# Optimization experiments

Hardware: AMD Instinct MI355X
Metric: run time of the kernel (lower is better)

Reference implementation:

```python
import jax, jax.numpy as jnp
import numpy as np

B, EVI, L, H, K, NL = 16, 5, 128, 768, 21, 3
SIGMA = 0.1

def _kernel_mus(n):
    mu = [1.0]
    bin_size = 2.0 / (n - 1)
    mu.append(1 - bin_size / 2)
    for i in range(1, n - 1):
        mu.append(mu[i] - bin_size)
    return mu

MU = np.asarray(_kernel_mus(K), dtype=np.float32)                      # [K]
SIG = np.asarray([0.001] + [SIGMA] * (K - 1), dtype=np.float32)        # [K]


def setup_inputs() -> dict:
    key = jax.random.key(0)
    ks = jax.random.split(key, 8)
    std = 0.02
    inputs_hiddens = jax.random.normal(ks[0], (B, EVI, L, H), jnp.float32)
    inputs = jax.random.normal(ks[1], (B, EVI, H), jnp.float32)
    # mask_text: valid tokens with CLS (position 0) zeroed, as in torch forward
    mask_text = jnp.ones((B, EVI, L), jnp.float32).at[:, :, 0].set(0.0)
    seg = (jnp.arange(L) >= L // 2).astype(jnp.float32)  # first half = claim, second = evidence
    mask_claim = (1.0 - seg) * mask_text
    mask_evidence = seg * mask_text
    return {
        "inputs_hiddens": inputs_hiddens,
        "inputs": inputs,
        "mask_text": mask_text,
        "mask_claim": mask_claim,
        "mask_evidence": mask_evidence,
        "W_att": jax.random.normal(ks[2], (K, 1), jnp.float32) * std,
        "b_att": jnp.zeros((1,), jnp.float32),
        "W_sel": jax.random.normal(ks[3], (K, 1), jnp.float32) * std,
        "b_sel": jnp.zeros((1,), jnp.float32),
        "gat_W1": jax.random.normal(ks[4], (2 * H, 128), jnp.float32) * std,
        "gat_b1": jnp.zeros((128,), jnp.float32),
        "gat_W2": jax.random.normal(ks[5], (128, 1), jnp.float32) * std,
        "gat_b2": jnp.zeros((1,), jnp.float32),
        "inf_W": jax.random.normal(ks[6], (2 * H, NL), jnp.float32) * std,
        "inf_b": jnp.zeros((NL,), jnp.float32),
    }


def _l2norm(x):
    # F.normalize(p=2, dim=-1) with eps=1e-12
    return x / jnp.maximum(jnp.linalg.norm(x, axis=-1, keepdims=True), 1e-12)


def _kernel_pool(sim, attn_d):
    # sim: [N, Lq, Ld]; attn_d: [N, Ld]  ->  [N, Lq, K]
    # exp(-(sim - mu)^2 / (2 sigma^2)) masked by doc attention, summed over doc tokens
    pv = jnp.exp(-((sim[..., None] - MU) ** 2) / (2.0 * SIG ** 2)) * attn_d[:, None, :, None]
    return pv.sum(axis=2)


def _intersect_att(qn, dn, attn_q, attn_d, W_att, b_att):
    # token-level attention scores over q tokens: [N, Lq]
    sim = jnp.einsum('nqh,ndh->nqd', qn, dn)
    lp = jnp.log(jnp.maximum(_kernel_pool(sim, attn_d), 1e-10))  # [N, Lq, K]
    lp = (lp @ W_att + b_att)[..., 0]                            # [N, Lq]
    lp = jnp.where(attn_q == 0.0, -1e4, lp)
    return jax.nn.softmax(lp, axis=1)


def _intersect_sel(qn, dn, attn_q, attn_d, W_sel, b_sel):
    # per-pair evidence selection logit: [N, 1]
    sim = jnp.einsum('nqh,ndh->nqd', qn, dn)
    lp = jnp.log(jnp.maximum(_kernel_pool(sim, attn_d), 1e-10)) * attn_q[..., None] * 0.01
    lp = lp.sum(axis=1) / (attn_q.sum(axis=1, keepdims=True) + 1e-10)  # [N, K]
    return lp @ W_sel + b_sel


def _gat(x, W1, b1, W2, b2):
    # proj_gat: Linear(2H,128) -> ReLU -> Linear(128,1)
    return jnp.maximum(x @ W1 + b1, 0.0) @ W2 + b2


def reference(inputs_hiddens, inputs, mask_text, mask_claim, mask_evidence,
              W_att, b_att, W_sel, b_sel, gat_W1, gat_b1, gat_W2, gat_b2,
              inf_W, inf_b):
    hid = inputs_hiddens                          # [B, EVI, L, H]
    hn = _l2norm(hid)
    hn_flat = hn.reshape(-1, L, H)

    # evidence selection prior over EVI pieces
    sel = _intersect_sel(hn_flat, hn_flat,
                         mask_claim.reshape(-1, L), mask_evidence.reshape(-1, L),
                         W_sel, b_sel)
    select_prob = jax.nn.softmax(sel.reshape(B, EVI, 1), axis=1)

    att_de = []
    for i in range(EVI):  # fixed small structural loop
        own_n = hn[:, i]                           # [B, L, H]
        own_mask = mask_text[:, i]                 # [B, L]
        dn = jnp.broadcast_to(own_n[:, None], (B, EVI, L, H)).reshape(-1, L, H)
        dm = jnp.broadcast_to(own_mask[:, None], (B, EVI, L)).reshape(-1, L)
        att = _intersect_att(hn_flat, dn, mask_evidence.reshape(-1, L), dm, W_att, b_att)
        att = att.reshape(B, EVI, L, 1)
        denoise = (att * hid).sum(axis=2)          # [B, EVI, H]
        own_inp = jnp.broadcast_to(inputs[:, i:i + 1], (B, EVI, H))
        w_de = jax.nn.softmax(_gat(jnp.concatenate([own_inp, denoise], -1),
                                   gat_W1, gat_b1, gat_W2, gat_b2), axis=1)  # [B, EVI, 1]
        att_de.append((denoise * w_de).sum(axis=1))  # [B, H]

    att_de = jnp.stack(att_de, axis=1)             # [B, EVI, H]
    feats = jnp.concatenate([inputs, att_de], axis=-1)  # [B, EVI, 2H]
    class_prob = jax.nn.softmax(feats @ inf_W + inf_b, axis=2)
    prob = jnp.log((select_prob * class_prob).sum(axis=1))  # [B, NL]
    return prob
```

## Files before the change

### kernel.cpp

```cpp
#include <hip/hip_runtime.h>
#include <math.h>

#define NB 16
#define NE 5
#define LL 128
#define HH 768
#define NK 21
#define NCLS 3
#define NN (NB*NE)

typedef float f32x4 __attribute__((ext_vector_type(4)));
typedef float f32x8 __attribute__((ext_vector_type(8)));
typedef short s16x8 __attribute__((ext_vector_type(8)));

__device__ __forceinline__ short bf16rne(float f) {
    union { float f; unsigned u; } c; c.f = f;
    unsigned u = c.u;
    unsigned r = (u + 0x7FFFu + ((u >> 16) & 1u)) >> 16;
    return (short)r;
}
__device__ __forceinline__ float sum8(f32x8 x) {
    return ((x[0] + x[1]) + (x[2] + x[3])) + ((x[4] + x[5]) + (x[6] + x[7]));
}
__device__ __forceinline__ f32x8 exp2v(f32x8 x) {
    f32x8 r;
    r[0] = exp2f(x[0]); r[1] = exp2f(x[1]); r[2] = exp2f(x[2]); r[3] = exp2f(x[3]);
    r[4] = exp2f(x[4]); r[5] = exp2f(x[5]); r[6] = exp2f(x[6]); r[7] = exp2f(x[7]);
    return r;
}
__device__ __forceinline__ f32x8 mk8(float4 a, float4 b) {
    f32x8 r;
    r[0] = a.x; r[1] = a.y; r[2] = a.z; r[3] = a.w;
    r[4] = b.x; r[5] = b.y; r[6] = b.z; r[7] = b.w;
    return r;
}
__device__ __forceinline__ float dot4(float4 a, float4 b) {
    return fmaf(a.x, b.x, fmaf(a.y, b.y, fmaf(a.z, b.z, a.w * b.w)));
}

__global__ __launch_bounds__(256) void k_prep(const float* __restrict__ hid,
                                              short* __restrict__ hswz,
                                              const float* __restrict__ W1,
                                              float* __restrict__ w1t) {
    __shared__ float sT[64][65];
    const int tid = threadIdx.x;
    if (blockIdx.x >= 640) {
        const int bb = blockIdx.x - 640;
        const int tI = bb >> 1, jI = bb & 1;
        #pragma unroll
        for (int i = 0; i < 16; ++i) {
            const int r = (tid >> 6) + i * 4, c = tid & 63;
            sT[r][c] = W1[(size_t)(tI * 64 + r) * 128 + jI * 64 + c];
        }
        __syncthreads();
        #pragma unroll
        for (int i = 0; i < 16; ++i) {
            const int r = (tid >> 6) + i * 4, c = tid & 63;
            w1t[(size_t)(jI * 64 + r) * 1536 + tI * 64 + c] = sT[c][r];
        }
        return;
    }
    const int n = blockIdx.x >> 3, slab = blockIdx.x & 7;
    const int l = tid & 63, w = tid >> 6;
    float* sInv = &sT[0][0];
    #pragma unroll
    for (int rr = 0; rr < 4; ++rr) {
        const int lr = w * 4 + rr;
        const int row = slab * 16 + lr;
        const float4* rp = reinterpret_cast<const float4*>(hid + ((size_t)n * LL + row) * HH);
        float4 a = rp[l], b = rp[l + 64], c = rp[l + 128];
        float ss = a.x*a.x + a.y*a.y + a.z*a.z + a.w*a.w
                 + b.x*b.x + b.y*b.y + b.z*b.z + b.w*b.w
                 + c.x*c.x + c.y*c.y + c.z*c.z + c.w*c.w;
        #pragma unroll
        for (int o = 32; o > 0; o >>= 1) ss += __shfl_xor(ss, o, 64);
        if (l == 0) sInv[lr] = 1.0f / fmaxf(sqrtf(ss), 1e-12f);
    }
    __syncthreads();
    const float* base = hid + (size_t)n * LL * HH;
    s16x8* dst = reinterpret_cast<s16x8*>(hswz) + (size_t)n * 12288;
    #pragma unroll
    for (int i = 0; i < 6; ++i) {
        const int uid = i * 256 + tid;
        const int s = uid >> 6, sub = uid & 63;
        const int r15 = sub >> 2, kc = sub & 3;
        const int row = slab * 16 + r15;
        const int k0 = s * 32 + kc * 8;
        const float4* p = reinterpret_cast<const float4*>(base + (size_t)row * HH + k0);
        float4 v0 = p[0], v1 = p[1];
        const float inv = sInv[r15];
        s16x8 h;
        h[0] = bf16rne(v0.x * inv); h[1] = bf16rne(v0.y * inv);
        h[2] = bf16rne(v0.z * inv); h[3] = bf16rne(v0.w * inv);
        h[4] = bf16rne(v1.x * inv); h[5] = bf16rne(v1.y * inv);
        h[6] = bf16rne(v1.z * inv); h[7] = bf16rne(v1.w * inv);
        dst[(size_t)s * 512 + slab * 64 + kc * 16 + r15] = h;
    }
}

__global__ __launch_bounds__(256, 3) void k_simpool(
    const short* __restrict__ hswz,
    const float* __restrict__ mask_text, const float* __restrict__ mask_claim,
    const float* __restrict__ mask_evidence,
    const float* __restrict__ W_att, const float* __restrict__ b_att,
    const float* __restrict__ W_sel,
    float* __restrict__ attw, float2* __restrict__ dselPart)
{
    const int bid = blockIdx.x;
    const int b = bid & 15, rest = bid >> 4;
    const int pair = rest >> 1, qh = rest & 1;
    const int e = pair / NE, ep = pair - e * NE;
    const int nq = b * NE + e, nd = b * NE + ep;
    const bool diag = (e == ep);
    const int tid = threadIdx.x, lane = tid & 63, w = tid >> 6;
    const int lx = lane & 15, lg = lane >> 4;

    __shared__ s16x8 sB[1024];
    __shared__ __align__(16) float sMT[LL];
    __shared__ __align__(16) float sMEd[LL];
    __shared__ float sMEq[64], sMCq[64], sSel[64];
    __shared__ float sWA[NK], sWS[NK], sCK[NK];

    if (tid < 128) {
        sMT[tid]  = mask_text[nd * LL + tid];
        sMEd[tid] = mask_evidence[nd * LL + tid];
    } else if (tid < 192) {
        const int q = tid - 128;
        sMEq[q] = mask_evidence[nq * LL + qh * 64 + q];
        sMCq[q] = mask_claim[nq * LL + qh * 64 + q];
    } else if (tid < 192 + NK) {
        sWA[tid - 192] = W_att[tid - 192] * 0.69314718f;
    } else if (tid < 213 + NK) {
        sWS[tid - 213] = W_sel[tid - 213] * 0.69314718f;
    } else if (tid < 254) {
        const int k = tid - 233;
        const float kk = (float)(k - 1);
        sCK[k] = exp2f(fmaf(kk, 13.7056029f, fmaf(kk * kk, -0.72134752f, -32.0f)));
    } else if (tid == 254) {
        sCK[0] = 1.0f;
    }

    const s16x8* gA = reinterpret_cast<const s16x8*>(hswz) + (size_t)nq * 12288;
    const s16x8* gB = reinterpret_cast<const s16x8*>(hswz) + (size_t)nd * 12288;

    {
        s16x8 p0 = gB[tid], p1 = gB[tid + 256], p2 = gB[tid + 512], p3 = gB[tid + 768];
        sB[tid] = p0; sB[tid + 256] = p1; sB[tid + 512] = p2; sB[tid + 768] = p3;
    }
    s16x8 b0 = gB[1024 + tid], b1 = gB[1024 + tid + 256],
          b2 = gB[1024 + tid + 512], b3 = gB[1024 + tid + 768];
    const int arow = (qh * 4 + w) * 64 + lane;
    s16x8 aC0 = gA[arow];
    s16x8 aC1 = gA[512 + arow];
    s16x8 aN0 = gA[1024 + arow];
    s16x8 aN1 = gA[1024 + 512 + arow];

    f32x4 acc[8];
    #pragma unroll
    for (int nj = 0; nj < 8; ++nj) acc[nj] = (f32x4){0.f, 0.f, 0.f, 0.f};

    for (int s = 0; s < 12; ++s) {
        __syncthreads();
        #pragma unroll
        for (int nj = 0; nj < 8; ++nj)
            acc[nj] = __builtin_amdgcn_mfma_f32_16x16x32_bf16(aC0, sB[nj * 64 + lane], acc[nj], 0, 0, 0);
        #pragma unroll
        for (int nj = 0; nj < 8; ++nj)
            acc[nj] = __builtin_amdgcn_mfma_f32_16x16x32_bf16(aC1, sB[512 + nj * 64 + lane], acc[nj], 0, 0, 0);
        if (s < 11) {
            __syncthreads();
            sB[tid] = b0; sB[tid + 256] = b1; sB[tid + 512] = b2; sB[tid + 768] = b3;
            aC0 = aN0; aC1 = aN1;
            if (s < 10) {
                const s16x8* gBs = gB + (s + 2) * 1024;
                b0 = gBs[tid]; b1 = gBs[tid + 256];
                b2 = gBs[tid + 512]; b3 = gBs[tid + 768];
                aN0 = gA[(s + 2) * 1024 + arow];
                aN1 = gA[(s + 2) * 1024 + 512 + arow];
            }
        }
    }

    float* sS = reinterpret_cast<float*>(sB);
    const int rloc = (w << 3) | (lane & 7);
    const int slice = lane >> 3;
    const int xr = lane & 7;
    const float bAtt = b_att[0];
    const size_t obase = ((size_t)ep * NN + nq) * LL + qh * 64;

    #pragma unroll
    for (int ph = 0; ph < 2; ++ph) {
        __syncthreads();
        if ((w >> 1) == ph) {
            const int wl = w & 1;
            #pragma unroll
            for (int nj = 0; nj < 8; ++nj) {
                const int col = nj * 16 + lx;
                #pragma unroll
                for (int r = 0; r < 4; ++r) {
                    const int row = wl * 16 + lg * 4 + r;
                    const int unit = (col >> 2) ^ (row & 7);
                    sS[row * 128 + unit * 4 + (col & 3)] = acc[nj][r];
                }
            }
        }
        __syncthreads();

        const float4* rp4 = reinterpret_cast<const float4*>(sS + rloc * 128);
        float pk[NK], vkk[NK];
        #pragma unroll
        for (int k = 0; k < NK; ++k) { pk[k] = 0.f; vkk[k] = 0.f; }

        #pragma unroll
        for (int c = 0; c < 2; ++c) {
            const float4 qa = rp4[(slice * 4 + c * 2) ^ xr];
            const float4 qb = rp4[(slice * 4 + c * 2 + 1) ^ xr];
            const f32x8 s = mk8(qa, qb);
            const int j0 = slice * 16 + c * 8;
            const f32x8 m = mk8(*reinterpret_cast<const float4*>(&sMT[j0]),
                                *reinterpret_cast<const float4*>(&sMT[j0 + 4]));
            f32x8 d = s - 1.0f;
            const f32x8 g = exp2v(d * d * -721347.52f);
            pk[0] += sum8(m * g);
            const f32x8 t = exp2v(s * -14.4269504f);
            d = s - 0.95f;
            const f32x8 P = exp2v(d * d * -72.134752f + 32.0f);
            f32x8 u = m * P;
            pk[1] += sum8(u);
            #pragma unroll
            for (int k = 2; k <= 20; ++k) { u *= t; pk[k] += sum8(u); }
            if (diag) {
                const f32x8 me = mk8(*reinterpret_cast<const float4*>(&sMEd[j0]),
                                     *reinterpret_cast<const float4*>(&sMEd[j0 + 4]));
                f32x8 uv = me * P;
                vkk[0] += sum8(me * g);
                vkk[1] += sum8(uv);
                #pragma unroll
                for (int k = 2; k <= 20; ++k) { uv *= t; vkk[k] += sum8(uv); }
            }
        }
        #pragma unroll
        for (int k = 0; k < NK; ++k) {
            pk[k] += __shfl_xor(pk[k], 8, 64);
            pk[k] += __shfl_xor(pk[k], 16, 64);
            pk[k] += __shfl_xor(pk[k], 32, 64);
        }
        if (diag) {
            #pragma unroll
            for (int k = 0; k < NK; ++k) {
                vkk[k] += __shfl_xor(vkk[k], 8, 64);
                vkk[k] += __shfl_xor(vkk[k], 16, 64);
                vkk[k] += __shfl_xor(vkk[k], 32, 64);
            }
        }
        const int grow = ph * 32 + rloc;
        float lgt = bAtt;
        #pragma unroll
        for (int k = 0; k < NK; ++k)
            lgt = fmaf(sWA[k], log2f(fmaxf(pk[k] * sCK[k], 1e-10f)), lgt);
        if (slice == 0)
            attw[obase + grow] = (sMEq[grow] == 0.0f) ? -10000.0f : lgt;
        if (diag) {
            float rv = 0.f;
            #pragma unroll
            for (int k = 0; k < NK; ++k)
                rv = fmaf(sWS[k], log2f(fmaxf(vkk[k] * sCK[k], 1e-10f)), rv);
            if (slice == 0) sSel[grow] = sMCq[grow] * rv;
        }
    }
    if (diag) {
        __syncthreads();
        if (tid < 64) {
            float su = sSel[tid], ms = sMCq[tid];
            #pragma unroll
            for (int o = 32; o > 0; o >>= 1) {
                su += __shfl_xor(su, o, 64);
                ms += __shfl_xor(ms, o, 64);
            }
            if (tid == 0) dselPart[nq * 2 + qh] = make_float2(su, ms);
        }
    }
}

__global__ __launch_bounds__(256) void k_denoise(
    const float* __restrict__ hid, const float* __restrict__ attw,
    float* __restrict__ denoi)
{
    const int blk = blockIdx.x;
    const int nq = blk / 3, ch = blk - nq * 3;
    const int tid = threadIdx.x, l = tid & 63, w = tid >> 6;
    __shared__ float sA[NE][LL];
    for (int ep = w; ep < NE; ep += 4) {
        const float* ap = attw + ((size_t)ep * NN + nq) * LL;
        float a0 = ap[l], a1 = ap[l + 64];
        float m = fmaxf(a0, a1);
        #pragma unroll
        for (int o = 32; o > 0; o >>= 1) m = fmaxf(m, __shfl_xor(m, o, 64));
        float e0 = __expf(a0 - m), e1 = __expf(a1 - m);
        float s = e0 + e1;
        #pragma unroll
        for (int o = 32; o > 0; o >>= 1) s += __shfl_xor(s, o, 64);
        float inv = 1.0f / s;
        sA[ep][l] = e0 * inv;
        sA[ep][l + 64] = e1 * inv;
    }
    __syncthreads();
    const int h = ch * 256 + tid;
    const float* hp = hid + (size_t)nq * LL * HH + h;
    float a0 = 0.f, a1 = 0.f, a2 = 0.f, a3 = 0.f, a4 = 0.f;
    #pragma unroll 8
    for (int q = 0; q < LL; ++q) {
        float x = hp[(size_t)q * HH];
        a0 = fmaf(sA[0][q], x, a0);
        a1 = fmaf(sA[1][q], x, a1);
        a2 = fmaf(sA[2][q], x, a2);
        a3 = fmaf(sA[3][q], x, a3);
        a4 = fmaf(sA[4][q], x, a4);
    }
    denoi[((size_t)0 * NN + nq) * HH + h] = a0;
    denoi[((size_t)1 * NN + nq) * HH + h] = a1;
    denoi[((size_t)2 * NN + nq) * HH + h] = a2;
    denoi[((size_t)3 * NN + nq) * HH + h] = a3;
    denoi[((size_t)4 * NN + nq) * HH + h] = a4;
}

__global__ __launch_bounds__(256) void k_gat2(
    const float* __restrict__ inputs, const float* __restrict__ denoise,
    const float* __restrict__ w1t, const float* __restrict__ b1,
    const float* __restrict__ W2, float* __restrict__ part)
{
    const int wid = blockIdx.x * 4 + (threadIdx.x >> 6);
    const int l = threadIdx.x & 63;
    const int jp = wid & 63;
    const int po = wid >> 6;
    const int j0 = jp * 2, j1 = j0 + 1;
    const int pb = po * 8;

    const float4* wc0 = reinterpret_cast<const float4*>(w1t + (size_t)j0 * 1536) + l;
    const float4* wc1 = reinterpret_cast<const float4*>(w1t + (size_t)j1 * 1536) + l;
    const float4* fin[8]; const float4* fde[8];
    #pragma unroll
    for (int u = 0; u < 8; ++u) {
        const int p = pb + u;
        const int i = p / NN; const int n2 = p - i * NN; const int bb = n2 / NE;
        fin[u] = reinterpret_cast<const float4*>(inputs + ((size_t)bb * NE + i) * HH) + l;
        fde[u] = reinterpret_cast<const float4*>(denoise + (size_t)p * HH) + l;
    }
    float a0[8], a1[8];
    #pragma unroll
    for (int u = 0; u < 8; ++u) { a0[u] = 0.f; a1[u] = 0.f; }

    #pragma unroll
    for (int it = 0; it < 3; ++it) {
        const float4 w0v = wc0[it * 64], w1v = wc1[it * 64];
        #pragma unroll
        for (int u = 0; u < 8; ++u) {
            const float4 f = fin[u][it * 64];
            a0[u] += dot4(f, w0v);
            a1[u] += dot4(f, w1v);
        }
    }
    #pragma unroll
    for (int it = 0; it < 3; ++it) {
        const float4 w0v = wc0[192 + it * 64], w1v = wc1[192 + it * 64];
        #pragma unroll
        for (int u = 0; u < 8; ++u) {
            const float4 f = fde[u][it * 64];
            a0[u] += dot4(f, w0v);
            a1[u] += dot4(f, w1v);
        }
    }
    #pragma unroll
    for (int u = 0; u < 8; ++u) {
        #pragma unroll
        for (int o = 32; o > 0; o >>= 1) {
            a0[u] += __shfl_xor(a0[u], o, 64);
            a1[u] += __shfl_xor(a1[u], o, 64);
        }
    }
    const float bb0 = b1[j0], bb1 = b1[j1], w20 = W2[j0], w21 = W2[j1];
    if (l == 0) {
        #pragma unroll
        for (int u = 0; u < 8; ++u) {
            float v = fmaxf(a0[u] + bb0, 0.f) * w20 + fmaxf(a1[u] + bb1, 0.f) * w21;
            part[(size_t)(pb + u) * 64 + jp] = v;
        }
    }
}

__global__ __launch_bounds__(256) void k_logits(
    const float* __restrict__ inputs, const float* __restrict__ denoise,
    const float* __restrict__ part, const float* __restrict__ inf_W,
    const float* __restrict__ inf_b, float* __restrict__ logi)
{
    const int bid = blockIdx.x;
    const int b = bid / NE, i = bid - b * NE;
    const int tid = threadIdx.x, l = tid & 63, wv = tid >> 6;
    __shared__ float sG[NE];
    for (int e2 = wv; e2 < NE; e2 += 4) {
        float v = part[(size_t)(i * NN + b * NE + e2) * 64 + l];
        #pragma unroll
        for (int o = 32; o > 0; o >>= 1) v += __shfl_xor(v, o, 64);
        if (l == 0) sG[e2] = v;
    }
    __syncthreads();
    float g0 = sG[0], g1 = sG[1], g2 = sG[2], g3 = sG[3], g4 = sG[4];
    float mm = fmaxf(fmaxf(fmaxf(g0, g1), fmaxf(g2, g3)), g4);
    float w0 = __expf(g0 - mm), w1 = __expf(g1 - mm), w2 = __expf(g2 - mm);
    float w3 = __expf(g3 - mm), w4 = __expf(g4 - mm);
    float inv = 1.0f / (w0 + w1 + w2 + w3 + w4);
    w0 *= inv; w1 *= inv; w2 *= inv; w3 *= inv; w4 *= inv;

    float p0 = 0.f, p1 = 0.f, p2 = 0.f;
    const float* xin = inputs + ((size_t)b * NE + i) * HH;
    const float* de = denoise + ((size_t)i * NN + b * NE) * HH;
    #pragma unroll
    for (int it = 0; it < 3; ++it) {
        int t = it * 256 + tid;
        float f = xin[t];
        p0 += f * inf_W[t * 3]; p1 += f * inf_W[t * 3 + 1]; p2 += f * inf_W[t * 3 + 2];
    }
    #pragma unroll
    for (int it = 0; it < 3; ++it) {
        int h = it * 256 + tid;
        float a = w0 * de[h] + w1 * de[HH + h] + w2 * de[2 * HH + h]
                + w3 * de[3 * HH + h] + w4 * de[4 * HH + h];
        int t = HH + h;
        p0 += a * inf_W[t * 3]; p1 += a * inf_W[t * 3 + 1]; p2 += a * inf_W[t * 3 + 2];
    }
    #pragma unroll
    for (int o = 32; o > 0; o >>= 1) {
        p0 += __shfl_xor(p0, o, 64);
        p1 += __shfl_xor(p1, o, 64);
        p2 += __shfl_xor(p2, o, 64);
    }
    __shared__ float red[4][NCLS];
    if (l == 0) { red[wv][0] = p0; red[wv][1] = p1; red[wv][2] = p2; }
    __syncthreads();
    if (tid < NCLS) {
        logi[bid * NCLS + tid] = red[0][tid] + red[1][tid] + red[2][tid] + red[3][tid]
                               + inf_b[tid];
    }
}

__global__ __launch_bounds__(64) void k_combine(
    const float2* __restrict__ dselPart, const float* __restrict__ b_sel,
    const float* __restrict__ logi, float* __restrict__ out)
{
    const int b = threadIdx.x;
    if (b >= NB) return;
    const float bs = b_sel[0];
    float d0, d1, d2, d3, d4;
#define DSEL(I, D) { float2 pa = dselPart[(b * NE + (I)) * 2], pb = dselPart[(b * NE + (I)) * 2 + 1]; \
                     (D) = bs + 0.01f * (pa.x + pb.x) / ((pa.y + pb.y) + 1e-10f); }
    DSEL(0, d0) DSEL(1, d1) DSEL(2, d2) DSEL(3, d3) DSEL(4, d4)
#undef DSEL
    float m = fmaxf(fmaxf(fmaxf(d0, d1), fmaxf(d2, d3)), d4);
    float s0 = __expf(d0 - m), s1 = __expf(d1 - m), s2 = __expf(d2 - m);
    float s3 = __expf(d3 - m), s4 = __expf(d4 - m);
    float sinv = 1.0f / (s0 + s1 + s2 + s3 + s4);
    float sp0 = s0 * sinv, sp1 = s1 * sinv, sp2 = s2 * sinv, sp3 = s3 * sinv, sp4 = s4 * sinv;
    float acc0 = 0.f, acc1 = 0.f, acc2 = 0.f;
#define CMB(I, SP) { \
        float l0 = logi[(b * NE + (I)) * NCLS], l1 = logi[(b * NE + (I)) * NCLS + 1], \
              l2 = logi[(b * NE + (I)) * NCLS + 2]; \
        float mm = fmaxf(fmaxf(l0, l1), l2); \
        float e0 = __expf(l0 - mm), e1 = __expf(l1 - mm), e2 = __expf(l2 - mm); \
        float si = 1.0f / (e0 + e1 + e2); \
        acc0 += (SP) * e0 * si; acc1 += (SP) * e1 * si; acc2 += (SP) * e2 * si; }
    CMB(0, sp0) CMB(1, sp1) CMB(2, sp2) CMB(3, sp3) CMB(4, sp4)
#undef CMB
    out[b * NCLS + 0] = logf(acc0);
    out[b * NCLS + 1] = logf(acc1);
    out[b * NCLS + 2] = logf(acc2);
}

extern "C" void kernel_launch(void* const* d_in, const int* in_sizes, int n_in,
                              void* d_out, int out_size, void* d_ws, size_t ws_size,
                              hipStream_t stream) {
    (void)in_sizes; (void)n_in; (void)out_size; (void)ws_size;
    const float* hid           = (const float*)d_in[0];
    const float* inputs        = (const float*)d_in[1];
    const float* mask_text     = (const float*)d_in[2];
    const float* mask_claim    = (const float*)d_in[3];
    const float* mask_evidence = (const float*)d_in[4];
    const float* W_att  = (const float*)d_in[5];
    const float* b_att  = (const float*)d_in[6];
    const float* W_sel  = (const float*)d_in[7];
    const float* b_sel  = (const float*)d_in[8];
    const float* gat_W1 = (const float*)d_in[9];
    const float* gat_b1 = (const float*)d_in[10];
    const float* gat_W2 = (const float*)d_in[11];
    const float* gat_b2 = (const float*)d_in[12];
    const float* inf_W  = (const float*)d_in[13];
    const float* inf_b  = (const float*)d_in[14];
    (void)gat_b2;

    short* hswz  = (short*)d_ws;
    float* denoi = (float*)((char*)d_ws + 15728640);
    float* attw  = denoi + 307200;
    float2* dselPart = (float2*)(attw + 51200);
    float* w1t   = (float*)(dselPart + 160);
    float* part  = w1t + 196608;
    float* logi  = part + 25600;

    k_prep<<<688, 256, 0, stream>>>(hid, hswz, gat_W1, w1t);
    k_simpool<<<800, 256, 0, stream>>>(hswz, mask_text, mask_claim, mask_evidence,
                                       W_att, b_att, W_sel, attw, dselPart);
    k_denoise<<<NN * 3, 256, 0, stream>>>(hid, attw, denoi);
    k_gat2<<<800, 256, 0, stream>>>(inputs, denoi, w1t, gat_b1, gat_W2, part);
    k_logits<<<NN, 256, 0, stream>>>(inputs, denoi, part, inf_W, inf_b, logi);
    k_combine<<<1, 64, 0, stream>>>(dselPart, b_sel, logi, (float*)d_out);
}
```

Before: 92.77 us.

## Retile simpool MFMA to 2x4 wave grid with double-buffered LDS; fuse logits+combine

The similarity GEMM in k_simpool now uses a 2x2 wave layout where each wave computes 2 row tiles by 4 column tiles, so every B fragment read from LDS feeds two MFMAs. K is split into 24 steps of 32 with a double-buffered 16KB LDS B tile, which needs one barrier per step instead of two. The launch-bounds occupancy hint drops from 3 to 2 blocks per CU. Separately, k_logits and k_combine are merged into one 16-block kernel, removing a launch, at the cost of less parallelism in the final stage.

```diff
diff --git a/kernel.cpp b/kernel.cpp
--- a/kernel.cpp
+++ b/kernel.cpp
@@ -98,7 +98,7 @@
     }
 }
 
-__global__ __launch_bounds__(256, 3) void k_simpool(
+__global__ __launch_bounds__(256, 2) void k_simpool(
     const short* __restrict__ hswz,
     const float* __restrict__ mask_text, const float* __restrict__ mask_claim,
     const float* __restrict__ mask_evidence,
@@ -114,8 +114,9 @@
     const bool diag = (e == ep);
     const int tid = threadIdx.x, lane = tid & 63, w = tid >> 6;
     const int lx = lane & 15, lg = lane >> 4;
-
-    __shared__ s16x8 sB[1024];
+    const int rw = w & 1, cw = w >> 1;
+
+    __shared__ s16x8 sB[2][512];
     __shared__ __align__(16) float sMT[LL];
     __shared__ __align__(16) float sMEd[LL];
     __shared__ float sMEq[64], sMCq[64], sSel[64];
@@ -143,41 +144,41 @@
     const s16x8* gA = reinterpret_cast<const s16x8*>(hswz) + (size_t)nq * 12288;
     const s16x8* gB = reinterpret_cast<const s16x8*>(hswz) + (size_t)nd * 12288;
 
-    {
-        s16x8 p0 = gB[tid], p1 = gB[tid + 256], p2 = gB[tid + 512], p3 = gB[tid + 768];
-        sB[tid] = p0; sB[tid + 256] = p1; sB[tid + 512] = p2; sB[tid + 768] = p3;
-    }
-    s16x8 b0 = gB[1024 + tid], b1 = gB[1024 + tid + 256],
-          b2 = gB[1024 + tid + 512], b3 = gB[1024 + tid + 768];
-    const int arow = (qh * 4 + w) * 64 + lane;
-    s16x8 aC0 = gA[arow];
-    s16x8 aC1 = gA[512 + arow];
-    s16x8 aN0 = gA[1024 + arow];
-    s16x8 aN1 = gA[1024 + 512 + arow];
-
-    f32x4 acc[8];
-    #pragma unroll
-    for (int nj = 0; nj < 8; ++nj) acc[nj] = (f32x4){0.f, 0.f, 0.f, 0.f};
-
-    for (int s = 0; s < 12; ++s) {
-        __syncthreads();
-        #pragma unroll
-        for (int nj = 0; nj < 8; ++nj)
-            acc[nj] = __builtin_amdgcn_mfma_f32_16x16x32_bf16(aC0, sB[nj * 64 + lane], acc[nj], 0, 0, 0);
-        #pragma unroll
-        for (int nj = 0; nj < 8; ++nj)
-            acc[nj] = __builtin_amdgcn_mfma_f32_16x16x32_bf16(aC1, sB[512 + nj * 64 + lane], acc[nj], 0, 0, 0);
-        if (s < 11) {
+    const int rt0 = (qh * 4 + rw * 2) * 64;
+    const int rt1 = rt0 + 64;
+    const int cb  = cw * 256;
+
+    sB[0][tid] = gB[tid];
+    sB[0][tid + 256] = gB[tid + 256];
+    s16x8 a0 = gA[rt0 + lane], a1 = gA[rt1 + lane];
+
+    f32x4 acc[2][4];
+    #pragma unroll
+    for (int mi = 0; mi < 2; ++mi)
+        #pragma unroll
+        for (int j = 0; j < 4; ++j) acc[mi][j] = (f32x4){0.f, 0.f, 0.f, 0.f};
+
+    __syncthreads();
+
+    for (int s = 0; s < 24; ++s) {
+        const int cur = s & 1;
+        s16x8 nB0, nB1, n0, n1;
+        if (s < 23) {
+            const s16x8* gBs = gB + (s + 1) * 512;
+            nB0 = gBs[tid]; nB1 = gBs[tid + 256];
+            const s16x8* gAs = gA + (s + 1) * 512;
+            n0 = gAs[rt0 + lane]; n1 = gAs[rt1 + lane];
+        }
+        #pragma unroll
+        for (int j = 0; j < 4; ++j) {
+            s16x8 bf = sB[cur][cb + j * 64 + lane];
+            acc[0][j] = __builtin_amdgcn_mfma_f32_16x16x32_bf16(a0, bf, acc[0][j], 0, 0, 0);
+            acc[1][j] = __builtin_amdgcn_mfma_f32_16x16x32_bf16(a1, bf, acc[1][j], 0, 0, 0);
+        }
+        if (s < 23) {
+            sB[1 - cur][tid] = nB0; sB[1 - cur][tid + 256] = nB1;
+            a0 = n0; a1 = n1;
             __syncthreads();
-            sB[tid] = b0; sB[tid + 256] = b1; sB[tid + 512] = b2; sB[tid + 768] = b3;
-            aC0 = aN0; aC1 = aN1;
-            if (s < 10) {
-                const s16x8* gBs = gB + (s + 2) * 1024;
-                b0 = gBs[tid]; b1 = gBs[tid + 256];
-                b2 = gBs[tid + 512]; b3 = gBs[tid + 768];
-                aN0 = gA[(s + 2) * 1024 + arow];
-                aN1 = gA[(s + 2) * 1024 + 512 + arow];
-            }
         }
     }
 
@@ -191,16 +192,18 @@
     #pragma unroll
     for (int ph = 0; ph < 2; ++ph) {
         __syncthreads();
-        if ((w >> 1) == ph) {
-            const int wl = w & 1;
+        if (rw == ph) {
             #pragma unroll
-            for (int nj = 0; nj < 8; ++nj) {
-                const int col = nj * 16 + lx;
+            for (int mi = 0; mi < 2; ++mi) {
                 #pragma unroll
-                for (int r = 0; r < 4; ++r) {
-                    const int row = wl * 16 + lg * 4 + r;
-                    const int unit = (col >> 2) ^ (row & 7);
-                    sS[row * 128 + unit * 4 + (col & 3)] = acc[nj][r];
+                for (int j = 0; j < 4; ++j) {
+                    const int col = cw * 64 + j * 16 + lx;
+                    #pragma unroll
+                    for (int r = 0; r < 4; ++r) {
+                        const int row = mi * 16 + lg * 4 + r;
+                        const int unit = (col >> 2) ^ (row & 7);
+                        sS[row * 128 + unit * 4 + (col & 3)] = acc[mi][j][r];
+                    }
                 }
             }
         }
@@ -388,91 +391,92 @@
     }
 }
 
-__global__ __launch_bounds__(256) void k_logits(
+__global__ __launch_bounds__(256) void k_final16(
     const float* __restrict__ inputs, const float* __restrict__ denoise,
     const float* __restrict__ part, const float* __restrict__ inf_W,
-    const float* __restrict__ inf_b, float* __restrict__ logi)
+    const float* __restrict__ inf_b, const float2* __restrict__ dselPart,
+    const float* __restrict__ b_sel, float* __restrict__ out)
 {
-    const int bid = blockIdx.x;
-    const int b = bid / NE, i = bid - b * NE;
+    const int b = blockIdx.x;
     const int tid = threadIdx.x, l = tid & 63, wv = tid >> 6;
-    __shared__ float sG[NE];
-    for (int e2 = wv; e2 < NE; e2 += 4) {
+    __shared__ float sGat[NE][NE];
+    __shared__ float sLogi[NE][NCLS];
+    __shared__ float red[4][NCLS];
+
+    for (int idx = wv; idx < NE * NE; idx += 4) {
+        const int i = idx / NE, e2 = idx - i * NE;
         float v = part[(size_t)(i * NN + b * NE + e2) * 64 + l];
         #pragma unroll
         for (int o = 32; o > 0; o >>= 1) v += __shfl_xor(v, o, 64);
-        if (l == 0) sG[e2] = v;
+        if (l == 0) sGat[i][e2] = v;
     }
     __syncthreads();
-    float g0 = sG[0], g1 = sG[1], g2 = sG[2], g3 = sG[3], g4 = sG[4];
-    float mm = fmaxf(fmaxf(fmaxf(g0, g1), fmaxf(g2, g3)), g4);
-    float w0 = __expf(g0 - mm), w1 = __expf(g1 - mm), w2 = __expf(g2 - mm);
-    float w3 = __expf(g3 - mm), w4 = __expf(g4 - mm);
-    float inv = 1.0f / (w0 + w1 + w2 + w3 + w4);
-    w0 *= inv; w1 *= inv; w2 *= inv; w3 *= inv; w4 *= inv;
-
-    float p0 = 0.f, p1 = 0.f, p2 = 0.f;
-    const float* xin = inputs + ((size_t)b * NE + i) * HH;
-    const float* de = denoise + ((size_t)i * NN + b * NE) * HH;
-    #pragma unroll
-    for (int it = 0; it < 3; ++it) {
-        int t = it * 256 + tid;
-        float f = xin[t];
-        p0 += f * inf_W[t * 3]; p1 += f * inf_W[t * 3 + 1]; p2 += f * inf_W[t * 3 + 2];
-    }
-    #pragma unroll
-    for (int it = 0; it < 3; ++it) {
-        int h = it * 256 + tid;
-        float a = w0 * de[h] + w1 * de[HH + h] + w2 * de[2 * HH + h]
-                + w3 * de[3 * HH + h] + w4 * de[4 * HH + h];
-        int t = HH + h;
-        p0 += a * inf_W[t * 3]; p1 += a * inf_W[t * 3 + 1]; p2 += a * inf_W[t * 3 + 2];
-    }
-    #pragma unroll
-    for (int o = 32; o > 0; o >>= 1) {
-        p0 += __shfl_xor(p0, o, 64);
-        p1 += __shfl_xor(p1, o, 64);
-        p2 += __shfl_xor(p2, o, 64);
-    }
-    __shared__ float red[4][NCLS];
-    if (l == 0) { red[wv][0] = p0; red[wv][1] = p1; red[wv][2] = p2; }
-    __syncthreads();
-    if (tid < NCLS) {
-        logi[bid * NCLS + tid] = red[0][tid] + red[1][tid] + red[2][tid] + red[3][tid]
-                               + inf_b[tid];
-    }
-}
-
-__global__ __launch_bounds__(64) void k_combine(
-    const float2* __restrict__ dselPart, const float* __restrict__ b_sel,
-    const float* __restrict__ logi, float* __restrict__ out)
-{
-    const int b = threadIdx.x;
-    if (b >= NB) return;
-    const float bs = b_sel[0];
-    float d0, d1, d2, d3, d4;
+
+    for (int i = 0; i < NE; ++i) {
+        float g0 = sGat[i][0], g1 = sGat[i][1], g2 = sGat[i][2],
+              g3 = sGat[i][3], g4 = sGat[i][4];
+        float mm = fmaxf(fmaxf(fmaxf(g0, g1), fmaxf(g2, g3)), g4);
+        float w0 = __expf(g0 - mm), w1 = __expf(g1 - mm), w2 = __expf(g2 - mm);
+        float w3 = __expf(g3 - mm), w4 = __expf(g4 - mm);
+        float inv = 1.0f / (w0 + w1 + w2 + w3 + w4);
+        w0 *= inv; w1 *= inv; w2 *= inv; w3 *= inv; w4 *= inv;
+
+        float p0 = 0.f, p1 = 0.f, p2 = 0.f;
+        const float* xin = inputs + ((size_t)b * NE + i) * HH;
+        const float* de = denoise + ((size_t)i * NN + b * NE) * HH;
+        #pragma unroll
+        for (int it = 0; it < 3; ++it) {
+            int t = it * 256 + tid;
+            float f = xin[t];
+            p0 += f * inf_W[t * 3]; p1 += f * inf_W[t * 3 + 1]; p2 += f * inf_W[t * 3 + 2];
+        }
+        #pragma unroll
+        for (int it = 0; it < 3; ++it) {
+            int h = it * 256 + tid;
+            float a = w0 * de[h] + w1 * de[HH + h] + w2 * de[2 * HH + h]
+                    + w3 * de[3 * HH + h] + w4 * de[4 * HH + h];
+            int t = HH + h;
+            p0 += a * inf_W[t * 3]; p1 += a * inf_W[t * 3 + 1]; p2 += a * inf_W[t * 3 + 2];
+        }
+        #pragma unroll
+        for (int o = 32; o > 0; o >>= 1) {
+            p0 += __shfl_xor(p0, o, 64);
+            p1 += __shfl_xor(p1, o, 64);
+            p2 += __shfl_xor(p2, o, 64);
+        }
+        if (l == 0) { red[wv][0] = p0; red[wv][1] = p1; red[wv][2] = p2; }
+        __syncthreads();
+        if (tid < NCLS)
+            sLogi[i][tid] = red[0][tid] + red[1][tid] + red[2][tid] + red[3][tid]
+                          + inf_b[tid];
+        __syncthreads();
+    }
+
+    if (tid == 0) {
+        const float bs = b_sel[0];
+        float d0, d1, d2, d3, d4;
 #define DSEL(I, D) { float2 pa = dselPart[(b * NE + (I)) * 2], pb = dselPart[(b * NE + (I)) * 2 + 1]; \
                      (D) = bs + 0.01f * (pa.x + pb.x) / ((pa.y + pb.y) + 1e-10f); }
-    DSEL(0, d0) DSEL(1, d1) DSEL(2, d2) DSEL(3, d3) DSEL(4, d4)
+        DSEL(0, d0) DSEL(1, d1) DSEL(2, d2) DSEL(3, d3) DSEL(4, d4)
 #undef DSEL
-    float m = fmaxf(fmaxf(fmaxf(d0, d1), fmaxf(d2, d3)), d4);
-    float s0 = __expf(d0 - m), s1 = __expf(d1 - m), s2 = __expf(d2 - m);
-    float s3 = __expf(d3 - m), s4 = __expf(d4 - m);
-    float sinv = 1.0f / (s0 + s1 + s2 + s3 + s4);
-    float sp0 = s0 * sinv, sp1 = s1 * sinv, sp2 = s2 * sinv, sp3 = s3 * sinv, sp4 = s4 * sinv;
-    float acc0 = 0.f, acc1 = 0.f, acc2 = 0.f;
-#define CMB(I, SP) { \
-        float l0 = logi[(b * NE + (I)) * NCLS], l1 = logi[(b * NE + (I)) * NCLS + 1], \
-              l2 = logi[(b * NE + (I)) * NCLS + 2]; \
-        float mm = fmaxf(fmaxf(l0, l1), l2); \
-        float e0 = __expf(l0 - mm), e1 = __expf(l1 - mm), e2 = __expf(l2 - mm); \
-        float si = 1.0f / (e0 + e1 + e2); \
-        acc0 += (SP) * e0 * si; acc1 += (SP) * e1 * si; acc2 += (SP) * e2 * si; }
-    CMB(0, sp0) CMB(1, sp1) CMB(2, sp2) CMB(3, sp3) CMB(4, sp4)
-#undef CMB
-    out[b * NCLS + 0] = logf(acc0);
-    out[b * NCLS + 1] = logf(acc1);
-    out[b * NCLS + 2] = logf(acc2);
+        float m = fmaxf(fmaxf(fmaxf(d0, d1), fmaxf(d2, d3)), d4);
+        float s0 = __expf(d0 - m), s1 = __expf(d1 - m), s2 = __expf(d2 - m);
+        float s3 = __expf(d3 - m), s4 = __expf(d4 - m);
+        float sinv = 1.0f / (s0 + s1 + s2 + s3 + s4);
+        float sp[NE] = { s0 * sinv, s1 * sinv, s2 * sinv, s3 * sinv, s4 * sinv };
+        float acc0 = 0.f, acc1 = 0.f, acc2 = 0.f;
+        #pragma unroll
+        for (int i = 0; i < NE; ++i) {
+            float l0 = sLogi[i][0], l1 = sLogi[i][1], l2 = sLogi[i][2];
+            float mm = fmaxf(fmaxf(l0, l1), l2);
+            float e0 = __expf(l0 - mm), e1 = __expf(l1 - mm), e2 = __expf(l2 - mm);
+            float si = 1.0f / (e0 + e1 + e2);
+            acc0 += sp[i] * e0 * si; acc1 += sp[i] * e1 * si; acc2 += sp[i] * e2 * si;
+        }
+        out[b * NCLS + 0] = logf(acc0);
+        out[b * NCLS + 1] = logf(acc1);
+        out[b * NCLS + 2] = logf(acc2);
+    }
 }
 
 extern "C" void kernel_launch(void* const* d_in, const int* in_sizes, int n_in,
@@ -502,13 +506,12 @@
     float2* dselPart = (float2*)(attw + 51200);
     float* w1t   = (float*)(dselPart + 160);
     float* part  = w1t + 196608;
-    float* logi  = part + 25600;
 
     k_prep<<<688, 256, 0, stream>>>(hid, hswz, gat_W1, w1t);
     k_simpool<<<800, 256, 0, stream>>>(hswz, mask_text, mask_claim, mask_evidence,
                                        W_att, b_att, W_sel, attw, dselPart);
     k_denoise<<<NN * 3, 256, 0, stream>>>(hid, attw, denoi);
     k_gat2<<<800, 256, 0, stream>>>(inputs, denoi, w1t, gat_b1, gat_W2, part);
-    k_logits<<<NN, 256, 0, stream>>>(inputs, denoi, part, inf_W, inf_b, logi);
-    k_combine<<<1, 64, 0, stream>>>(dselPart, b_sel, logi, (float*)d_out);
-}
+    k_final16<<<NB, 256, 0, stream>>>(inputs, denoi, part, inf_W, inf_b,
+                                      dselPart, b_sel, (float*)d_out);
+}
```

Measured after the change: 98.23 us. +5.9%, slower.
